# Performance work log

Hardware: AMD Instinct MI355X
Metric: run time of the kernel (lower is better)

The kernel has to match this reference:

```python
import jax, jax.numpy as jnp
import numpy as np

NB_KNN = (10, 20, 100, 200)   # values of k to evaluate; max_k = 200
T = 0.07                       # softmax temperature
NUM_CLASSES = 1000


def setup_inputs() -> dict:
    key = jax.random.key(0)
    k1, k2, k3 = jax.random.split(key, 3)
    features_rank = jax.random.normal(k1, (256, 512), jnp.float32)      # (B, d) query features
    train_features = jax.random.normal(k2, (100000, 512), jnp.float32)  # (N, d) train bank
    train_labels = jax.random.randint(k3, (100000,), 0, NUM_CLASSES)     # (N,) int labels
    return {"features_rank": features_rank, "train_features": train_features,
            "train_labels": train_labels}


def _knn_probs(features_rank, train_features, train_labels):
    max_k = max(NB_KNN)
    # similarity: (B, N) = (B, d) @ (d, N)  -- mirrors torch.mm(broadcasted, train_features_rank_T)
    sims = features_rank @ train_features.T
    topk_sims, idx = jax.lax.top_k(sims, max_k)          # (B, max_k), sorted descending
    neighbors = train_labels[idx]                         # (B, max_k) gathered labels
    w = jax.nn.softmax(topk_sims / T, axis=1)             # (B, max_k) neighbor weights
    B = features_rank.shape[0]
    rows = jnp.arange(B)[:, None]                         # (B, 1) row indices for scatter
    # Instead of materializing one_hot (B, max_k, C) and summing prefixes,
    # scatter-add the first k weights into per-class buckets (same math, fused).
    probs = [jnp.zeros((B, NUM_CLASSES), w.dtype).at[rows, neighbors[:, :k]].add(w[:, :k])
             for k in NB_KNN]
    return jnp.stack(probs, axis=0)                       # (len(NB_KNN), B, C)


def reference(features_rank, train_features, train_labels):
    return _knn_probs(features_rank, train_features, train_labels)
```

## Files before the change

kernel.cpp:

```cpp
#include <hip/hip_runtime.h>
#include <math.h>

#define KDIM   512
#define NCLS   1000
#define CUTOFF 3.0f
#define MAXCAP 4096
#define BN     64
#define BK     64
#define NSTAGE (KDIM / BK)

typedef __attribute__((ext_vector_type(8))) short  short8;
typedef __attribute__((ext_vector_type(4))) float  floatx4;

__device__ __forceinline__ unsigned enc_f(float f) {
    unsigned u = __float_as_uint(f);
    return (u & 0x80000000u) ? ~u : (u | 0x80000000u);
}
__device__ __forceinline__ float dec_f(unsigned k) {
    unsigned u = (k & 0x80000000u) ? (k & 0x7FFFFFFFu) : ~k;
    return __uint_as_float(u);
}
__device__ __forceinline__ unsigned short f2bf(float f) {
    unsigned u = __float_as_uint(f);
    u += 0x7FFFu + ((u >> 16) & 1u);
    return (unsigned short)(u >> 16);
}
__device__ __forceinline__ float bf2f(unsigned short h) {
    return __uint_as_float(((unsigned)h) << 16);
}

__global__ void k_prep(const float* __restrict__ A, unsigned short* __restrict__ af,
                       unsigned* __restrict__ cnt, unsigned* __restrict__ gmax, int Brows) {
    int t = blockIdx.x * blockDim.x + threadIdx.x;
    if (t < Brows) { cnt[t] = 0u; gmax[t] = enc_f(-3.0e38f); }
    if (t >= Brows * (KDIM / 8)) return;
    int r = t >> 6;
    int o = t & 63;
    int s16 = r >> 4, c = o >> 2, kq = o & 3;
    int lane = kq * 16 + (r & 15);
    const float* src = A + (size_t)r * KDIM + o * 8;
    size_t bhi = ((size_t)((s16 * 16 + c) * 2 + 0) * 64 + lane) * 8;
    size_t blo = ((size_t)((s16 * 16 + c) * 2 + 1) * 64 + lane) * 8;
#pragma unroll
    for (int j = 0; j < 8; ++j) {
        float f = src[j];
        unsigned short h = f2bf(f);
        af[bhi + j] = h;
        af[blo + j] = f2bf(f - bf2f(h));
    }
}

__global__ __launch_bounds__(512, 4) void k_gemm(
    const float* __restrict__ Bt,
    const unsigned short* __restrict__ af,
    float* __restrict__ cand_val, int* __restrict__ cand_idx,
    unsigned* __restrict__ cnt, unsigned* __restrict__ gmax,
    int N, int cap)
{
    __shared__ short8 BsH[512];
    __shared__ short8 BsL[512];

    const int tid  = threadIdx.x;
    const int lane = tid & 63;
    const int wid  = tid >> 6;
    const int colBase = blockIdx.x * BN;

    const int nl  = tid >> 3;
    const int k8  = (tid & 7) * 8;
    const int gcol = colBase + nl;
    const bool colok = (gcol < N);
    const float* bsrc = Bt + (size_t)gcol * KDIM + k8;
    const int chw = k8 >> 5;
    const int kqw = (k8 >> 3) & 3;
    const int ctw = (nl >> 4) & 3;
    const int fidw = chw * 4 + ctw;
    const int lfw  = kqw * 16 + (nl & 15);
    const int slotw = fidw * 64 + (lfw ^ (kqw * 2 + chw));

    floatx4 acc[2][4];
#pragma unroll
    for (int rt = 0; rt < 2; ++rt)
#pragma unroll
        for (int ct = 0; ct < 4; ++ct)
            acc[rt][ct] = (floatx4){0.f, 0.f, 0.f, 0.f};

    const float4 z4 = make_float4(0.f, 0.f, 0.f, 0.f);
    float4 p0 = colok ? *(const float4*)(bsrc)     : z4;
    float4 p1 = colok ? *(const float4*)(bsrc + 4) : z4;

    for (int s = 0; s < NSTAGE; ++s) {
        union { float4 v[2]; float f[8]; } P;
        union { short8 v; unsigned short u[8]; } H, L;
        P.v[0] = p0; P.v[1] = p1;
#pragma unroll
        for (int j = 0; j < 8; ++j) {
            unsigned short h = f2bf(P.f[j]);
            H.u[j] = h;
            L.u[j] = f2bf(P.f[j] - bf2f(h));
        }
        __syncthreads();
        BsH[slotw] = H.v;
        BsL[slotw] = L.v;
        __syncthreads();

        if (s + 1 < NSTAGE) {
            const float* nsrc = bsrc + (s + 1) * BK;
            p0 = colok ? *(const float4*)(nsrc)     : z4;
            p1 = colok ? *(const float4*)(nsrc + 4) : z4;
        }

#pragma unroll
        for (int chunk = 0; chunk < 2; ++chunk) {
            const int cg = s * 2 + chunk;
            short8 aH[2], aL[2];
#pragma unroll
            for (int rt = 0; rt < 2; ++rt) {
                const int s16 = wid * 2 + rt;
                size_t sl = (size_t)((s16 * 16 + cg) * 2) * 64 + lane;
                aH[rt] = *(const short8*)(af + sl * 8);
                aL[rt] = *(const short8*)(af + (sl + 64) * 8);
            }
            const int g = (lane >> 4) * 2 + chunk;
#pragma unroll
            for (int ct = 0; ct < 4; ++ct) {
                const int idx = (chunk * 4 + ct) * 64 + (lane ^ g);
                short8 bh = BsH[idx];
                short8 bl = BsL[idx];
#pragma unroll
                for (int rt = 0; rt < 2; ++rt) {
                    acc[rt][ct] = __builtin_amdgcn_mfma_f32_16x16x32_bf16(aH[rt], bh, acc[rt][ct], 0, 0, 0);
                    acc[rt][ct] = __builtin_amdgcn_mfma_f32_16x16x32_bf16(aH[rt], bl, acc[rt][ct], 0, 0, 0);
                    acc[rt][ct] = __builtin_amdgcn_mfma_f32_16x16x32_bf16(aL[rt], bh, acc[rt][ct], 0, 0, 0);
                }
            }
        }
    }

    const int q   = lane >> 4;
    const int n15 = lane & 15;
#pragma unroll
    for (int rt = 0; rt < 2; ++rt) {
#pragma unroll
        for (int reg = 0; reg < 4; ++reg) {
            const int row = wid * 32 + rt * 16 + q * 4 + reg;
            float m = fmaxf(fmaxf(acc[rt][0][reg], acc[rt][1][reg]),
                            fmaxf(acc[rt][2][reg], acc[rt][3][reg]));
#pragma unroll
            for (int off = 1; off < 16; off <<= 1) m = fmaxf(m, __shfl_xor(m, off));
            unsigned oldk = 0u;
            if (n15 == 0) oldk = atomicMax(&gmax[row], enc_f(m));
            oldk = (unsigned)__shfl((int)oldk, lane & 48);
            const float thr = fmaxf(dec_f(oldk), m) - CUTOFF;
#pragma unroll
            for (int ct = 0; ct < 4; ++ct) {
                const float v = acc[rt][ct][reg];
                const int col = colBase + ct * 16 + n15;
                if (v >= thr && col < N) {
                    unsigned p = atomicAdd(&cnt[row], 1u);
                    if (p < (unsigned)cap) {
                        cand_val[(size_t)row * cap + p] = v;
                        cand_idx[(size_t)row * cap + p] = col;
                    }
                }
            }
        }
    }
}

__global__ __launch_bounds__(256) void k_finalize(
    const float* __restrict__ cand_val,
    const int* __restrict__ cand_idx,
    const unsigned* __restrict__ cnt,
    const unsigned* __restrict__ gmax,
    const int* __restrict__ labels,
    float* __restrict__ out,
    int Brows, int cap)
{
    __shared__ float s_val[256];
    __shared__ int   s_idx[256];
    __shared__ int   s_n;
    const int row = blockIdx.x;
    const int tid = threadIdx.x;
    if (tid == 0) s_n = 0;
    __syncthreads();

    const float m   = dec_f(gmax[row]);
    const float thr = m - CUTOFF;
    const int n = min((int)cnt[row], cap);
    for (int i = tid; i < n; i += 256) {
        float v = cand_val[(size_t)row * cap + i];
        if (v >= thr) {
            int p = atomicAdd(&s_n, 1);
            if (p < 256) { s_val[p] = v; s_idx[p] = cand_idx[(size_t)row * cap + i]; }
        }
    }
    __syncthreads();

    for (int c = tid; c < 4 * NCLS; c += 256) {
        int s = c / NCLS, cc = c - s * NCLS;
        out[(size_t)s * ((size_t)Brows * NCLS) + (size_t)row * NCLS + cc] = 0.f;
    }
    __syncthreads();

    if (tid == 0) {
        int ns = min(s_n, 256);
        for (int i = 1; i < ns; ++i) {
            float v = s_val[i]; int ix = s_idx[i];
            int j = i - 1;
            while (j >= 0 && s_val[j] < v) { s_val[j+1] = s_val[j]; s_idx[j+1] = s_idx[j]; --j; }
            s_val[j+1] = v; s_idx[j+1] = ix;
        }
        if (ns > 200) ns = 200;
        float Z = 0.f;
        for (int i = 0; i < ns; ++i) Z += expf((s_val[i] - m) / 0.07f);
        float invZ = 1.f / Z;
        const int kv[4] = {10, 20, 100, 200};
        for (int i = 0; i < ns; ++i) {
            float w = expf((s_val[i] - m) / 0.07f) * invZ;
            int lab = labels[s_idx[i]];
#pragma unroll
            for (int s = 0; s < 4; ++s)
                if (i < kv[s])
                    out[(size_t)s * ((size_t)Brows * NCLS) + (size_t)row * NCLS + lab] += w;
        }
    }
}

extern "C" void kernel_launch(void* const* d_in, const int* in_sizes, int n_in,
                              void* d_out, int out_size, void* d_ws, size_t ws_size,
                              hipStream_t stream) {
    const float* A      = (const float*)d_in[0];
    const float* Bt     = (const float*)d_in[1];
    const int*   labels = (const int*)d_in[2];
    float* out = (float*)d_out;

    const int Brows = in_sizes[0] / KDIM;
    const int N     = in_sizes[2];

    size_t af_elems = (size_t)Brows * KDIM * 2;
    unsigned short* af = (unsigned short*)d_ws;
    unsigned* cnt  = (unsigned*)(af + af_elems);
    unsigned* gmax = cnt + Brows;
    char* rest = (char*)(gmax + Brows);
    size_t used  = (size_t)(rest - (char*)d_ws);
    size_t avail = (ws_size > used) ? (ws_size - used) : 0;
    int cap = (int)((avail / ((size_t)Brows * 8)) < (size_t)MAXCAP
                        ? (avail / ((size_t)Brows * 8)) : (size_t)MAXCAP);
    if (cap < 1) cap = 1;
    float* cand_val = (float*)rest;
    int*   cand_idx = (int*)(cand_val + (size_t)Brows * cap);

    k_prep<<<(Brows * (KDIM / 8) + 255) / 256, 256, 0, stream>>>(A, af, cnt, gmax, Brows);
    k_gemm<<<(N + BN - 1) / BN, 512, 0, stream>>>(Bt, af, cand_val, cand_idx, cnt, gmax, N, cap);
    k_finalize<<<Brows, 256, 0, stream>>>(cand_val, cand_idx, cnt, gmax, labels, out, Brows, cap);
}
```

Measured before the change: 398.3 us.

## Double-buffer B tile in LDS with two-stage register prefetch in GEMM

Splits the shared-memory B tiles into two buffers and prefetches global data two stages ahead. The next stage's bf16 split is converted and written to the alternate buffer while the current stage's MFMAs run. This replaces two barriers per stage with one. LDS use doubles (16KB per block) and register pressure rises from the extra prefetch registers, which may reduce occupancy under launch_bounds(512,4).

```diff
diff --git a/kernel.cpp b/kernel.cpp
--- a/kernel.cpp
+++ b/kernel.cpp
@@ -57,8 +57,8 @@
     unsigned* __restrict__ cnt, unsigned* __restrict__ gmax,
     int N, int cap)
 {
-    __shared__ short8 BsH[512];
-    __shared__ short8 BsL[512];
+    __shared__ short8 BsH[2][512];
+    __shared__ short8 BsL[2][512];
 
     const int tid  = threadIdx.x;
     const int lane = tid & 63;
@@ -85,28 +85,41 @@
             acc[rt][ct] = (floatx4){0.f, 0.f, 0.f, 0.f};
 
     const float4 z4 = make_float4(0.f, 0.f, 0.f, 0.f);
-    float4 p0 = colok ? *(const float4*)(bsrc)     : z4;
-    float4 p1 = colok ? *(const float4*)(bsrc + 4) : z4;
-
-    for (int s = 0; s < NSTAGE; ++s) {
+    float4 c0 = colok ? *(const float4*)(bsrc)          : z4;
+    float4 c1 = colok ? *(const float4*)(bsrc + 4)      : z4;
+    float4 n0 = colok ? *(const float4*)(bsrc + BK)     : z4;
+    float4 n1 = colok ? *(const float4*)(bsrc + BK + 4) : z4;
+
+    {
         union { float4 v[2]; float f[8]; } P;
         union { short8 v; unsigned short u[8]; } H, L;
-        P.v[0] = p0; P.v[1] = p1;
+        P.v[0] = c0; P.v[1] = c1;
 #pragma unroll
         for (int j = 0; j < 8; ++j) {
             unsigned short h = f2bf(P.f[j]);
-            H.u[j] = h;
-            L.u[j] = f2bf(P.f[j] - bf2f(h));
-        }
-        __syncthreads();
-        BsH[slotw] = H.v;
-        BsL[slotw] = L.v;
-        __syncthreads();
-
+            H.u[j] = h; L.u[j] = f2bf(P.f[j] - bf2f(h));
+        }
+        BsH[0][slotw] = H.v; BsL[0][slotw] = L.v;
+    }
+    __syncthreads();
+
+    for (int s = 0; s < NSTAGE; ++s) {
         if (s + 1 < NSTAGE) {
-            const float* nsrc = bsrc + (s + 1) * BK;
-            p0 = colok ? *(const float4*)(nsrc)     : z4;
-            p1 = colok ? *(const float4*)(nsrc + 4) : z4;
+            c0 = n0; c1 = n1;
+            if (s + 2 < NSTAGE) {
+                const float* p = bsrc + (s + 2) * BK;
+                n0 = colok ? *(const float4*)(p)     : z4;
+                n1 = colok ? *(const float4*)(p + 4) : z4;
+            }
+            union { float4 v[2]; float f[8]; } P;
+            union { short8 v; unsigned short u[8]; } H, L;
+            P.v[0] = c0; P.v[1] = c1;
+#pragma unroll
+            for (int j = 0; j < 8; ++j) {
+                unsigned short h = f2bf(P.f[j]);
+                H.u[j] = h; L.u[j] = f2bf(P.f[j] - bf2f(h));
+            }
+            BsH[(s + 1) & 1][slotw] = H.v; BsL[(s + 1) & 1][slotw] = L.v;
         }
 
 #pragma unroll
@@ -124,8 +137,8 @@
 #pragma unroll
             for (int ct = 0; ct < 4; ++ct) {
                 const int idx = (chunk * 4 + ct) * 64 + (lane ^ g);
-                short8 bh = BsH[idx];
-                short8 bl = BsL[idx];
+                short8 bh = BsH[s & 1][idx];
+                short8 bl = BsL[s & 1][idx];
 #pragma unroll
                 for (int rt = 0; rt < 2; ++rt) {
                     acc[rt][ct] = __builtin_amdgcn_mfma_f32_16x16x32_bf16(aH[rt], bh, acc[rt][ct], 0, 0, 0);
@@ -134,6 +147,7 @@
                 }
             }
         }
+        __syncthreads();
     }
 
     const int q   = lane >> 4;
```

Result: no change. 395.1 us (-0.8%).

## Drop LDS staging in GEMM; load B fragments directly into registers with double buffering

Applied to the files above, without the earlier changes.

The similarity GEMM no longer stages the train-feature tile through shared memory with two barriers per stage. Each wave now loads its own B fragments straight from global memory into registers, double-buffered one 32-wide k-chunk ahead, and converts them to bf16 hi/lo pairs itself. Blocks shrink to 256 threads and each wave covers 4 row tiles instead of 2, so each wave now handles 64 query rows against 64 columns. This removes LDS traffic and barriers. In exchange, all four waves redundantly load and convert the same B data, and more accumulator registers are live per thread, which may lower occupancy.

```diff
diff --git a/kernel.cpp b/kernel.cpp
--- a/kernel.cpp
+++ b/kernel.cpp
@@ -6,8 +6,7 @@
 #define CUTOFF 3.0f
 #define MAXCAP 4096
 #define BN     64
-#define BK     64
-#define NSTAGE (KDIM / BK)
+#define NCHUNK (KDIM / 32)
 
 typedef __attribute__((ext_vector_type(8))) short  short8;
 typedef __attribute__((ext_vector_type(4))) float  floatx4;
@@ -50,99 +49,93 @@
     }
 }
 
-__global__ __launch_bounds__(512, 4) void k_gemm(
+__global__ __launch_bounds__(256, 2) void k_gemm(
     const float* __restrict__ Bt,
     const unsigned short* __restrict__ af,
     float* __restrict__ cand_val, int* __restrict__ cand_idx,
     unsigned* __restrict__ cnt, unsigned* __restrict__ gmax,
     int N, int cap)
 {
-    __shared__ short8 BsH[512];
-    __shared__ short8 BsL[512];
-
     const int tid  = threadIdx.x;
     const int lane = tid & 63;
     const int wid  = tid >> 6;
     const int colBase = blockIdx.x * BN;
-
-    const int nl  = tid >> 3;
-    const int k8  = (tid & 7) * 8;
-    const int gcol = colBase + nl;
-    const bool colok = (gcol < N);
-    const float* bsrc = Bt + (size_t)gcol * KDIM + k8;
-    const int chw = k8 >> 5;
-    const int kqw = (k8 >> 3) & 3;
-    const int ctw = (nl >> 4) & 3;
-    const int fidw = chw * 4 + ctw;
-    const int lfw  = kqw * 16 + (nl & 15);
-    const int slotw = fidw * 64 + (lfw ^ (kqw * 2 + chw));
-
-    floatx4 acc[2][4];
-#pragma unroll
-    for (int rt = 0; rt < 2; ++rt)
+    const int q    = lane >> 4;
+    const int n15  = lane & 15;
+
+    const float* bp[4];
+#pragma unroll
+    for (int ct = 0; ct < 4; ++ct) {
+        int c = colBase + ct * 16 + n15;
+        if (c > N - 1) c = N - 1;
+        bp[ct] = Bt + (size_t)c * KDIM + q * 8;
+    }
+    const unsigned short* ap[4];
+#pragma unroll
+    for (int rt = 0; rt < 4; ++rt)
+        ap[rt] = af + (size_t)(wid * 4 + rt) * 16384 + lane * 8;
+
+    floatx4 acc[4][4];
+#pragma unroll
+    for (int rt = 0; rt < 4; ++rt)
 #pragma unroll
         for (int ct = 0; ct < 4; ++ct)
             acc[rt][ct] = (floatx4){0.f, 0.f, 0.f, 0.f};
 
-    const float4 z4 = make_float4(0.f, 0.f, 0.f, 0.f);
-    float4 p0 = colok ? *(const float4*)(bsrc)     : z4;
-    float4 p1 = colok ? *(const float4*)(bsrc + 4) : z4;
-
-    for (int s = 0; s < NSTAGE; ++s) {
-        union { float4 v[2]; float f[8]; } P;
-        union { short8 v; unsigned short u[8]; } H, L;
-        P.v[0] = p0; P.v[1] = p1;
-#pragma unroll
-        for (int j = 0; j < 8; ++j) {
-            unsigned short h = f2bf(P.f[j]);
-            H.u[j] = h;
-            L.u[j] = f2bf(P.f[j] - bf2f(h));
-        }
-        __syncthreads();
-        BsH[slotw] = H.v;
-        BsL[slotw] = L.v;
-        __syncthreads();
-
-        if (s + 1 < NSTAGE) {
-            const float* nsrc = bsrc + (s + 1) * BK;
-            p0 = colok ? *(const float4*)(nsrc)     : z4;
-            p1 = colok ? *(const float4*)(nsrc + 4) : z4;
-        }
-
-#pragma unroll
-        for (int chunk = 0; chunk < 2; ++chunk) {
-            const int cg = s * 2 + chunk;
-            short8 aH[2], aL[2];
-#pragma unroll
-            for (int rt = 0; rt < 2; ++rt) {
-                const int s16 = wid * 2 + rt;
-                size_t sl = (size_t)((s16 * 16 + cg) * 2) * 64 + lane;
-                aH[rt] = *(const short8*)(af + sl * 8);
-                aL[rt] = *(const short8*)(af + (sl + 64) * 8);
-            }
-            const int g = (lane >> 4) * 2 + chunk;
+    float4 Bf[2][4][2];
+#pragma unroll
+    for (int ct = 0; ct < 4; ++ct) {
+        Bf[0][ct][0] = *(const float4*)(bp[ct]);
+        Bf[0][ct][1] = *(const float4*)(bp[ct] + 4);
+    }
+
+#pragma unroll 2
+    for (int cg = 0; cg < NCHUNK; ++cg) {
+        const int cur = cg & 1, nxt = cur ^ 1;
+
+        short8 aH[4], aL[4];
+#pragma unroll
+        for (int rt = 0; rt < 4; ++rt) {
+            const unsigned short* p = ap[rt] + cg * 1024;
+            aH[rt] = *(const short8*)(p);
+            aL[rt] = *(const short8*)(p + 512);
+        }
+        if (cg < NCHUNK - 1) {
 #pragma unroll
             for (int ct = 0; ct < 4; ++ct) {
-                const int idx = (chunk * 4 + ct) * 64 + (lane ^ g);
-                short8 bh = BsH[idx];
-                short8 bl = BsL[idx];
-#pragma unroll
-                for (int rt = 0; rt < 2; ++rt) {
-                    acc[rt][ct] = __builtin_amdgcn_mfma_f32_16x16x32_bf16(aH[rt], bh, acc[rt][ct], 0, 0, 0);
-                    acc[rt][ct] = __builtin_amdgcn_mfma_f32_16x16x32_bf16(aH[rt], bl, acc[rt][ct], 0, 0, 0);
-                    acc[rt][ct] = __builtin_amdgcn_mfma_f32_16x16x32_bf16(aL[rt], bh, acc[rt][ct], 0, 0, 0);
-                }
-            }
-        }
-    }
-
-    const int q   = lane >> 4;
-    const int n15 = lane & 15;
-#pragma unroll
-    for (int rt = 0; rt < 2; ++rt) {
+                const float* p = bp[ct] + (cg + 1) * 32;
+                Bf[nxt][ct][0] = *(const float4*)(p);
+                Bf[nxt][ct][1] = *(const float4*)(p + 4);
+            }
+        }
+        short8 bh[4], bl[4];
+#pragma unroll
+        for (int ct = 0; ct < 4; ++ct) {
+            union { float4 v[2]; float f[8]; } P;
+            union { short8 v; unsigned short u[8]; } H, L;
+            P.v[0] = Bf[cur][ct][0]; P.v[1] = Bf[cur][ct][1];
+#pragma unroll
+            for (int j = 0; j < 8; ++j) {
+                unsigned short h = f2bf(P.f[j]);
+                H.u[j] = h; L.u[j] = f2bf(P.f[j] - bf2f(h));
+            }
+            bh[ct] = H.v; bl[ct] = L.v;
+        }
+#pragma unroll
+        for (int ct = 0; ct < 4; ++ct)
+#pragma unroll
+            for (int rt = 0; rt < 4; ++rt) {
+                acc[rt][ct] = __builtin_amdgcn_mfma_f32_16x16x32_bf16(aH[rt], bh[ct], acc[rt][ct], 0, 0, 0);
+                acc[rt][ct] = __builtin_amdgcn_mfma_f32_16x16x32_bf16(aH[rt], bl[ct], acc[rt][ct], 0, 0, 0);
+                acc[rt][ct] = __builtin_amdgcn_mfma_f32_16x16x32_bf16(aL[rt], bh[ct], acc[rt][ct], 0, 0, 0);
+            }
+    }
+
+#pragma unroll
+    for (int rt = 0; rt < 4; ++rt) {
 #pragma unroll
         for (int reg = 0; reg < 4; ++reg) {
-            const int row = wid * 32 + rt * 16 + q * 4 + reg;
+            const int row = (wid * 4 + rt) * 16 + q * 4 + reg;
             float m = fmaxf(fmaxf(acc[rt][0][reg], acc[rt][1][reg]),
                             fmaxf(acc[rt][2][reg], acc[rt][3][reg]));
 #pragma unroll
@@ -251,6 +244,6 @@
     int*   cand_idx = (int*)(cand_val + (size_t)Brows * cap);
 
     k_prep<<<(Brows * (KDIM / 8) + 255) / 256, 256, 0, stream>>>(A, af, cnt, gmax, Brows);
-    k_gemm<<<(N + BN - 1) / BN, 512, 0, stream>>>(Bt, af, cand_val, cand_idx, cnt, gmax, N, cap);
+    k_gemm<<<(N + BN - 1) / BN, 256, 0, stream>>>(Bt, af, cand_val, cand_idx, cnt, gmax, N, cap);
     k_finalize<<<Brows, 256, 0, stream>>>(cand_val, cand_idx, cnt, gmax, labels, out, Brows, cap);
 }
```

Measured after the change: 465.2 us. 16.8% more time.
